# Kernel tuning notes

Measured on AMD Instinct MI355X. Metric: run time of the kernel, lower is better.

The kernel has to match this reference:

```python
import jax, jax.numpy as jnp
import numpy as np

D_IN = 2048
D_OUT = 2048
NUM_HEADS = 16
HEAD_DIM = D_OUT // NUM_HEADS


def setup_inputs() -> dict:
    key = jax.random.key(0)
    ks = jax.random.split(key, 6)
    b, t = 2, 2048
    x = jax.random.normal(ks[0], (b, t, D_IN), dtype=jnp.float32)
    s = 0.02
    Wq = jax.random.normal(ks[1], (D_OUT, D_IN), dtype=jnp.float32) * s
    Wk = jax.random.normal(ks[2], (D_OUT, D_IN), dtype=jnp.float32) * s
    Wv = jax.random.normal(ks[3], (D_OUT, D_IN), dtype=jnp.float32) * s
    Wo = jax.random.normal(ks[4], (D_OUT, D_OUT), dtype=jnp.float32) * s
    bo = jnp.zeros((D_OUT,), dtype=jnp.float32)
    theta = (10000.0 ** (-jnp.arange(0, HEAD_DIM, 2, dtype=jnp.float32) / HEAD_DIM))
    return {"x": x, "Wq": Wq, "Wk": Wk, "Wv": Wv, "Wo": Wo, "bo": bo, "theta": theta}


def _rope(v, sin, cos):
    # v: [b, t, h, d]; split even/odd feature indices, rotate, concat halves
    ve, vo = v[..., ::2], v[..., 1::2]
    return jnp.concatenate([ve * cos - vo * sin, ve * sin + vo * cos], axis=-1)


def reference(x, Wq, Wk, Wv, Wo, bo, theta):
    b, t, _ = x.shape
    q = (x @ Wq.T).reshape(b, t, NUM_HEADS, HEAD_DIM)
    k = (x @ Wk.T).reshape(b, t, NUM_HEADS, HEAD_DIM)
    v = (x @ Wv.T).reshape(b, t, NUM_HEADS, HEAD_DIM)

    pos = jnp.arange(t, dtype=jnp.float32)[:, None]          # [t, 1]
    freq = pos * theta[None, :]                              # [t, d/2]
    sin = jnp.sin(freq)[None, :, None, :]                    # [1, t, 1, d/2]
    cos = jnp.cos(freq)[None, :, None, :]
    q = _rope(q, sin, cos)
    k = _rope(k, sin, cos)

    # [b, h, t, t]
    scores = jnp.einsum('bqhd,bkhd->bhqk', q, k)
    causal = jnp.triu(jnp.ones((t, t), dtype=bool), k=1)
    scores = jnp.where(causal[None, None], -jnp.inf, scores)
    attn = jax.nn.softmax(scores / jnp.sqrt(jnp.float32(HEAD_DIM)), axis=-1)

    ctx = jnp.einsum('bhqk,bkhd->bqhd', attn, v).reshape(b, t, D_OUT)
    return ctx @ Wo.T + bo
```

## Files before the change

kernel.cpp:

```cpp
#include <hip/hip_runtime.h>

typedef unsigned short ushortT;
typedef short short8 __attribute__((ext_vector_type(8)));
typedef float floatx4 __attribute__((ext_vector_type(4)));

#define D_MODEL 2048
#define HEAD_DIM 128
#define NUM_HEADS 16
#define SEQ 2048
#define BATCH 2
#define M_TOK (BATCH * SEQ)
#define QKV_ELEMS ((size_t)M_TOK * D_MODEL)
#define W_ELEMS ((size_t)D_MODEL * D_MODEL)

__device__ __forceinline__ float bf2f(ushortT h) {
    return __uint_as_float(((unsigned int)h) << 16);
}
__device__ __forceinline__ ushortT f2bf(float f) {
    unsigned int u = __float_as_uint(f);
    u = u + 0x7fffu + ((u >> 16) & 1u);
    return (ushortT)(u >> 16);
}

__device__ __forceinline__ void gload_lds16(const ushortT* g, short* lds_wave_base) {
    __builtin_amdgcn_global_load_lds(
        (const __attribute__((address_space(1))) unsigned int*)g,
        (__attribute__((address_space(3))) unsigned int*)lds_wave_base,
        16, 0, 0);
}

__global__ __launch_bounds__(256) void cvt_all(
    const float* __restrict__ x,  const float* __restrict__ wq,
    const float* __restrict__ wk, const float* __restrict__ wv,
    const float* __restrict__ wo,
    ushortT* __restrict__ xb,  ushortT* __restrict__ wqb,
    ushortT* __restrict__ wkb, ushortT* __restrict__ wvb,
    ushortT* __restrict__ wob)
{
    const size_t XC = QKV_ELEMS / 8;
    const size_t WC = W_ELEMS / 8;
    size_t c = (size_t)blockIdx.x * 256 + threadIdx.x;
    const float* s; ushortT* d;
    if (c < XC)              { s = x;  d = xb;  }
    else if ((c -= XC) < WC) { s = wq; d = wqb; }
    else if ((c -= WC) < WC) { s = wk; d = wkb; }
    else if ((c -= WC) < WC) { s = wv; d = wvb; }
    else     { c -= WC;        s = wo; d = wob; }
    const float* f = s + c * 8;
    floatx4 a = *(const floatx4*)f;
    floatx4 b = *(const floatx4*)(f + 4);
    short8 r;
    r[0] = (short)f2bf(a.x); r[1] = (short)f2bf(a.y);
    r[2] = (short)f2bf(a.z); r[3] = (short)f2bf(a.w);
    r[4] = (short)f2bf(b.x); r[5] = (short)f2bf(b.y);
    r[6] = (short)f2bf(b.z); r[7] = (short)f2bf(b.w);
    *(short8*)(d + c * 8) = r;
}

template<bool OUTF32>
__global__ __launch_bounds__(256) void gemm_bt(
    const ushortT* __restrict__ A,
    const ushortT* __restrict__ W0, const ushortT* __restrict__ W1,
    const ushortT* __restrict__ W2,
    void* C0, void* C1, void* C2, const float* __restrict__ bias)
{
    __shared__ short As[128 * 32];
    __shared__ short Bs[128 * 32];

    const int z = blockIdx.z;
    const ushortT* W = (z == 0) ? W0 : (z == 1 ? W1 : W2);
    void* C = (z == 0) ? C0 : (z == 1 ? C1 : C2);

    const int tid  = threadIdx.x;
    const int wave = tid >> 6;
    const int lane = tid & 63;
    const int lr   = lane & 15;
    const int quad = lane >> 4;
    const int wm   = (wave & 1) * 64;
    const int wn   = (wave >> 1) * 64;

    const int blockM = blockIdx.y * 128;
    const int blockN = blockIdx.x * 128;

    const int srow = tid >> 2;
    const int scol = (tid & 3) * 8;
    const ushortT* ag = A + (size_t)(blockM + srow) * D_MODEL + scol;
    const ushortT* wg = W + (size_t)(blockN + srow) * D_MODEL + scol;
    short* al = As + wave * 512;
    short* bl = Bs + wave * 512;

    floatx4 acc[4][4];
    #pragma unroll
    for (int i = 0; i < 4; i++)
        #pragma unroll
        for (int j = 0; j < 4; j++) acc[i][j] = (floatx4){0.f, 0.f, 0.f, 0.f};

    for (int kk = 0; kk < D_MODEL; kk += 32) {
        gload_lds16(ag + kk,                 al);
        gload_lds16(ag + kk + 64 * D_MODEL,  al + 64 * 32);
        gload_lds16(wg + kk,                 bl);
        gload_lds16(wg + kk + 64 * D_MODEL,  bl + 64 * 32);
        __syncthreads();

        short8 af[4], bf[4];
        #pragma unroll
        for (int s = 0; s < 4; s++) {
            af[s] = *(const short8*)&As[(wm + s * 16 + lr) * 32 + quad * 8];
            bf[s] = *(const short8*)&Bs[(wn + s * 16 + lr) * 32 + quad * 8];
        }
        #pragma unroll
        for (int sm = 0; sm < 4; sm++)
            #pragma unroll
            for (int sn = 0; sn < 4; sn++)
                acc[sm][sn] = __builtin_amdgcn_mfma_f32_16x16x32_bf16(
                    af[sm], bf[sn], acc[sm][sn], 0, 0, 0);
        __syncthreads();
    }

    #pragma unroll
    for (int sm = 0; sm < 4; sm++) {
        const int row = blockM + wm + sm * 16 + quad * 4;
        #pragma unroll
        for (int sn = 0; sn < 4; sn++) {
            const int col = blockN + wn + sn * 16 + lr;
            const float bval = bias ? bias[col] : 0.f;
            #pragma unroll
            for (int rr = 0; rr < 4; rr++) {
                const float val = acc[sm][sn][rr] + bval;
                if constexpr (OUTF32)
                    ((float*)C)[(size_t)(row + rr) * D_MODEL + col] = val;
                else
                    ((ushortT*)C)[(size_t)(row + rr) * D_MODEL + col] = f2bf(val);
            }
        }
    }
}

__global__ __launch_bounds__(256) void rope_kernel(
    ushortT* __restrict__ qb, ushortT* __restrict__ kb,
    const float* __restrict__ theta)
{
    const int tok = blockIdx.x;
    ushortT* p = (blockIdx.y ? kb : qb) + (size_t)tok * D_MODEL;
    const int t = tok & (SEQ - 1);
    const int tid = threadIdx.x;
    const int d = tid & 63;
    const int hb = tid >> 6;

    const float fr = (float)t * theta[d];
    const float s = sinf(fr);
    const float c = cosf(fr);

    float ve[4], vo[4];
    #pragma unroll
    for (int i = 0; i < 4; i++) {
        ushortT* ph = p + (i * 4 + hb) * HEAD_DIM;
        ve[i] = bf2f(ph[2 * d]);
        vo[i] = bf2f(ph[2 * d + 1]);
    }
    __syncthreads();
    #pragma unroll
    for (int i = 0; i < 4; i++) {
        ushortT* ph = p + (i * 4 + hb) * HEAD_DIM;
        ph[d]      = f2bf(ve[i] * c - vo[i] * s);
        ph[d + 64] = f2bf(ve[i] * s + vo[i] * c);
    }
}

__global__ __launch_bounds__(256) void kpack_kernel(
    const ushortT* __restrict__ k, ushortT* __restrict__ kf)
{
    const int kt16 = blockIdx.x;
    const int bh   = blockIdx.y;
    const int b = bh >> 4, h = bh & 15;
    const int tid = threadIdx.x;
    const int ks = tid >> 6, lane = tid & 63;
    const int lr = lane & 15, quad = lane >> 4;
    short8 v = *(const short8*)(
        k + (size_t)(b * SEQ + kt16 * 16 + lr) * D_MODEL + h * HEAD_DIM + ks * 32 + quad * 8);
    *(short8*)(kf + ((size_t)(bh * 128 + kt16) * 4 + ks) * 512 + lane * 8) = v;
}

__global__ __launch_bounds__(256) void vpack_kernel(
    const ushortT* __restrict__ v, ushortT* __restrict__ vf)
{
    __shared__ ushortT tile[32][136];
    const int ct = blockIdx.x;
    const int bh = blockIdx.y;
    const int b = bh >> 4, h = bh & 15;
    const int tid = threadIdx.x;

    const int tt = tid >> 3;
    const int dc = (tid & 7) * 16;
    const ushortT* src = v + (size_t)(b * SEQ + ct * 32 + tt) * D_MODEL + h * HEAD_DIM + dc;
    *(short8*)&tile[tt][dc]     = *(const short8*)src;
    *(short8*)&tile[tt][dc + 8] = *(const short8*)(src + 8);
    __syncthreads();

    const int w = tid >> 6, lane = tid & 63;
    const int lr = lane & 15, quad = lane >> 4;
    #pragma unroll
    for (int p = 0; p < 2; p++) {
        const int rt = w + p * 4;
        short8 out;
        #pragma unroll
        for (int j = 0; j < 8; j++)
            out[j] = (short)tile[quad * 8 + j][rt * 16 + lr];
        *(short8*)(vf + ((size_t)(bh * 8 + rt) * 64 + ct) * 512 + lane * 8) = out;
    }
}

__global__ __launch_bounds__(256) void flash_attn2(
    const ushortT* __restrict__ q, const ushortT* __restrict__ kf,
    const ushortT* __restrict__ vf, ushortT* __restrict__ ctx)
{
    __shared__ short Kt[2][16 * 512];
    __shared__ short Vt[2][16 * 512];
    __shared__ short Pl[4][16][72];

    const unsigned lid = blockIdx.x;
    const int xcd  = lid & 7;
    const int slot = lid >> 3;
    const int ih   = slot >> 4;
    const int qtb  = slot & 15;
    const int bh   = (ih << 3) | xcd;

    const int b = bh >> 4, h = bh & 15;
    const size_t base = (size_t)b * SEQ * D_MODEL + h * HEAD_DIM;
    const size_t kfb = (size_t)bh * 128 * 4 * 512;
    const size_t vfb = (size_t)bh * 8 * 64 * 512;
    const int tid = threadIdx.x;
    const int w = tid >> 6, lane = tid & 63;
    const int lr = lane & 15, quad = lane >> 4;
    short* myP = &Pl[w][0][0];

    short8 onesf;
    #pragma unroll
    for (int j = 0; j < 8; j++) onesf[j] = (short)0x3F80;

    auto stage_tile = [&](int kt0, int buf) {
        const ushortT* ksrc = kf + kfb + (size_t)kt0 * 128;
        #pragma unroll
        for (int c = 0; c < 4; c++)
            gload_lds16(ksrc + c * 2048 + tid * 8, &Kt[buf][c * 2048 + w * 512]);
        #pragma unroll
        for (int c = 0; c < 4; c++) {
            const int e    = c * 2048 + tid * 8;
            const int dsub = e >> 10;
            const int rem  = e & 1023;
            const ushortT* vsrc = vf + vfb +
                ((size_t)dsub * 64 + (kt0 >> 5) + (rem >> 9)) * 512 + (rem & 511);
            gload_lds16(vsrc, &Vt[buf][c * 2048 + w * 512]);
        }
    };

    for (int pass = 0; pass < 2; pass++) {
        const int qt = (pass == 0) ? qtb : (SEQ / 64 - 1 - qtb);
        const int q0 = qt * 64 + w * 16;

        short8 Qf[4];
        {
            const ushortT* qrow = q + base + (size_t)(q0 + lr) * D_MODEL + quad * 8;
            #pragma unroll
            for (int ks = 0; ks < 4; ks++) {
                short8 raw = *(const short8*)(qrow + ks * 32);
                #pragma unroll
                for (int j = 0; j < 8; j++)
                    Qf[ks][j] = (short)f2bf(bf2f((ushortT)raw[j]) * 0.08838834764831845f);
            }
        }

        floatx4 Of[8];
        #pragma unroll
        for (int i = 0; i < 8; i++) Of[i] = (floatx4){0.f, 0.f, 0.f, 0.f};
        floatx4 lacc = (floatx4){0.f, 0.f, 0.f, 0.f};

        stage_tile(0, 0);
        asm volatile("s_waitcnt vmcnt(0)" ::: "memory");
        __builtin_amdgcn_s_barrier();
        asm volatile("" ::: "memory");

        const int ntiles = qt + 1;
        for (int t = 0; t < ntiles; ++t) {
            const int buf = t & 1;
            const int kt0 = t * 64;

            floatx4 Sf[4];
            #pragma unroll
            for (int sub = 0; sub < 4; sub++) {
                floatx4 acc = {0.f, 0.f, 0.f, 0.f};
                #pragma unroll
                for (int ks = 0; ks < 4; ks++) {
                    short8 Kf_ = *(const short8*)(&Kt[buf][(sub * 4 + ks) * 512 + lane * 8]);
                    acc = __builtin_amdgcn_mfma_f32_16x16x32_bf16(Qf[ks], Kf_, acc, 0, 0, 0);
                }
                Sf[sub] = acc;
            }

            if (kt0 == qt * 64) {
                #pragma unroll
                for (int sub = 0; sub < 4; sub++) {
                    const int ktg = kt0 + sub * 16 + lr;
                    #pragma unroll
                    for (int i = 0; i < 4; i++)
                        if (ktg > q0 + quad * 4 + i) Sf[sub][i] = -1e30f;
                }
            }

            #pragma unroll
            for (int sub = 0; sub < 4; sub++) {
                #pragma unroll
                for (int i = 0; i < 4; i++) {
                    const float p = __expf(fminf(Sf[sub][i], 60.f));
                    myP[(quad * 4 + i) * 72 + sub * 16 + lr] = (short)f2bf(p);
                }
            }

            short8 Vr[16];
            #pragma unroll
            for (int dsub = 0; dsub < 8; dsub++) {
                Vr[2 * dsub]     = *(const short8*)(&Vt[buf][dsub * 1024 + lane * 8]);
                Vr[2 * dsub + 1] = *(const short8*)(&Vt[buf][dsub * 1024 + 512 + lane * 8]);
            }

            if (t + 1 < ntiles) stage_tile((t + 1) * 64, buf ^ 1);

            asm volatile("s_waitcnt lgkmcnt(0)" ::: "memory");
            short8 Pf0 = *(const short8*)(myP + lr * 72 + quad * 8);
            short8 Pf1 = *(const short8*)(myP + lr * 72 + 32 + quad * 8);

            lacc = __builtin_amdgcn_mfma_f32_16x16x32_bf16(Pf0, onesf, lacc, 0, 0, 0);
            lacc = __builtin_amdgcn_mfma_f32_16x16x32_bf16(Pf1, onesf, lacc, 0, 0, 0);

            #pragma unroll
            for (int dsub = 0; dsub < 8; dsub++) {
                Of[dsub] = __builtin_amdgcn_mfma_f32_16x16x32_bf16(
                    Pf0, Vr[2 * dsub], Of[dsub], 0, 0, 0);
                Of[dsub] = __builtin_amdgcn_mfma_f32_16x16x32_bf16(
                    Pf1, Vr[2 * dsub + 1], Of[dsub], 0, 0, 0);
            }

            asm volatile("s_waitcnt vmcnt(0)" ::: "memory");
            __builtin_amdgcn_s_barrier();
            asm volatile("" ::: "memory");
        }

        float inv[4];
        #pragma unroll
        for (int i = 0; i < 4; i++) inv[i] = 1.f / lacc[i];
        #pragma unroll
        for (int dsub = 0; dsub < 8; dsub++)
            #pragma unroll
            for (int i = 0; i < 4; i++)
                ctx[base + (size_t)(q0 + quad * 4 + i) * D_MODEL + dsub * 16 + lr] =
                    f2bf(Of[dsub][i] * inv[i]);
    }
}

extern "C" void kernel_launch(void* const* d_in, const int* in_sizes, int n_in,
                              void* d_out, int out_size, void* d_ws, size_t ws_size,
                              hipStream_t stream) {
    const float* x     = (const float*)d_in[0];
    const float* Wq    = (const float*)d_in[1];
    const float* Wk    = (const float*)d_in[2];
    const float* Wv    = (const float*)d_in[3];
    const float* Wo    = (const float*)d_in[4];
    const float* bo    = (const float*)d_in[5];
    const float* theta = (const float*)d_in[6];

    ushortT* ws  = (ushortT*)d_ws;
    ushortT* qb  = ws;
    ushortT* kb  = ws + QKV_ELEMS;
    ushortT* vb  = ws + 2 * QKV_ELEMS;
    ushortT* kfb = ws + 3 * QKV_ELEMS;
    ushortT* xb  = kfb;
    ushortT* wqb = ws + 4 * QKV_ELEMS;
    ushortT* wkb = wqb + W_ELEMS;
    ushortT* wvb = wkb + W_ELEMS;
    ushortT* wob = wvb + W_ELEMS;

    cvt_all<<<dim3((unsigned)((QKV_ELEMS / 8 + 4 * (W_ELEMS / 8)) / 256)), 256, 0, stream>>>(
        x, Wq, Wk, Wv, Wo, xb, wqb, wkb, wvb, wob);

    gemm_bt<false><<<dim3(D_MODEL / 128, M_TOK / 128, 3), 256, 0, stream>>>(
        xb, wqb, wkb, wvb, qb, kb, vb, nullptr);

    rope_kernel<<<dim3(M_TOK, 2), 256, 0, stream>>>(qb, kb, theta);

    kpack_kernel<<<dim3(SEQ / 16, BATCH * NUM_HEADS), 256, 0, stream>>>(kb, kfb);

    vpack_kernel<<<dim3(SEQ / 32, BATCH * NUM_HEADS), 256, 0, stream>>>(vb, kb);

    flash_attn2<<<dim3(512), 256, 0, stream>>>(qb, kfb, kb, vb);

    gemm_bt<true><<<dim3(D_MODEL / 128, M_TOK / 128, 1), 256, 0, stream>>>(
        vb, wob, wob, wob, d_out, d_out, d_out, bo);
}
```

Baseline: 403.1 us.

## Fuse RoPE into K packing and Q load, write V fragments from GEMM

Removes the standalone rope and vpack kernels. RoPE is now applied to K inside kpack and to Q while flash attention loads its Q fragments, and the QKV GEMM epilogue writes V straight into the packed fragment layout. The GEMM also moves to a 64-wide K step with an XOR-swizzled LDS layout, which halves the number of barriers per K loop and is meant to reduce bank conflicts. The cost is sin/cos recomputed per element in kpack and flash attention, plus scattered 2-byte stores in the V epilogue.

Measured after the change: 441.7 us. +9.6%, slower.

```diff
diff --git a/kernel.cpp b/kernel.cpp
--- a/kernel.cpp
+++ b/kernel.cpp
@@ -57,15 +57,15 @@
     *(short8*)(d + c * 8) = r;
 }
 
-template<bool OUTF32>
+template<bool OUTF32, bool VFRAG>
 __global__ __launch_bounds__(256) void gemm_bt(
     const ushortT* __restrict__ A,
     const ushortT* __restrict__ W0, const ushortT* __restrict__ W1,
     const ushortT* __restrict__ W2,
     void* C0, void* C1, void* C2, const float* __restrict__ bias)
 {
-    __shared__ short As[128 * 32];
-    __shared__ short Bs[128 * 32];
+    __shared__ short As[128 * 64];
+    __shared__ short Bs[128 * 64];
 
     const int z = blockIdx.z;
     const ushortT* W = (z == 0) ? W0 : (z == 1 ? W1 : W2);
@@ -82,12 +82,15 @@
     const int blockM = blockIdx.y * 128;
     const int blockN = blockIdx.x * 128;
 
-    const int srow = tid >> 2;
-    const int scol = (tid & 3) * 8;
-    const ushortT* ag = A + (size_t)(blockM + srow) * D_MODEL + scol;
-    const ushortT* wg = W + (size_t)(blockN + srow) * D_MODEL + scol;
+    const int srow = tid >> 3;
+    const int scol = (tid & 7) * 8;
+    const int scolSwz = scol ^ ((srow & 7) << 3);
+    const ushortT* ag = A + (size_t)(blockM + srow) * D_MODEL + scolSwz;
+    const ushortT* wg = W + (size_t)(blockN + srow) * D_MODEL + scolSwz;
     short* al = As + wave * 512;
     short* bl = Bs + wave * 512;
+
+    const int rswz = (lr & 7) << 3;
 
     floatx4 acc[4][4];
     #pragma unroll
@@ -95,31 +98,36 @@
         #pragma unroll
         for (int j = 0; j < 4; j++) acc[i][j] = (floatx4){0.f, 0.f, 0.f, 0.f};
 
-    for (int kk = 0; kk < D_MODEL; kk += 32) {
-        gload_lds16(ag + kk,                 al);
-        gload_lds16(ag + kk + 64 * D_MODEL,  al + 64 * 32);
-        gload_lds16(wg + kk,                 bl);
-        gload_lds16(wg + kk + 64 * D_MODEL,  bl + 64 * 32);
+    for (int kk = 0; kk < D_MODEL; kk += 64) {
+        #pragma unroll
+        for (int i = 0; i < 4; i++) {
+            gload_lds16(ag + kk + (size_t)(i * 32) * D_MODEL, al + i * 2048);
+            gload_lds16(wg + kk + (size_t)(i * 32) * D_MODEL, bl + i * 2048);
+        }
         __syncthreads();
 
-        short8 af[4], bf[4];
-        #pragma unroll
-        for (int s = 0; s < 4; s++) {
-            af[s] = *(const short8*)&As[(wm + s * 16 + lr) * 32 + quad * 8];
-            bf[s] = *(const short8*)&Bs[(wn + s * 16 + lr) * 32 + quad * 8];
-        }
-        #pragma unroll
-        for (int sm = 0; sm < 4; sm++)
-            #pragma unroll
-            for (int sn = 0; sn < 4; sn++)
-                acc[sm][sn] = __builtin_amdgcn_mfma_f32_16x16x32_bf16(
-                    af[sm], bf[sn], acc[sm][sn], 0, 0, 0);
+        #pragma unroll
+        for (int kh = 0; kh < 2; kh++) {
+            const int cbase = (kh * 32 + quad * 8) ^ rswz;
+            short8 af[4], bf[4];
+            #pragma unroll
+            for (int s = 0; s < 4; s++) {
+                af[s] = *(const short8*)&As[(wm + s * 16 + lr) * 64 + cbase];
+                bf[s] = *(const short8*)&Bs[(wn + s * 16 + lr) * 64 + cbase];
+            }
+            #pragma unroll
+            for (int sm = 0; sm < 4; sm++)
+                #pragma unroll
+                for (int sn = 0; sn < 4; sn++)
+                    acc[sm][sn] = __builtin_amdgcn_mfma_f32_16x16x32_bf16(
+                        af[sm], bf[sn], acc[sm][sn], 0, 0, 0);
+        }
         __syncthreads();
     }
 
     #pragma unroll
     for (int sm = 0; sm < 4; sm++) {
-        const int row = blockM + wm + sm * 16 + quad * 4;
+        const int row0 = blockM + wm + sm * 16 + quad * 4;
         #pragma unroll
         for (int sn = 0; sn < 4; sn++) {
             const int col = blockN + wn + sn * 16 + lr;
@@ -127,48 +135,28 @@
             #pragma unroll
             for (int rr = 0; rr < 4; rr++) {
                 const float val = acc[sm][sn][rr] + bval;
-                if constexpr (OUTF32)
-                    ((float*)C)[(size_t)(row + rr) * D_MODEL + col] = val;
-                else
-                    ((ushortT*)C)[(size_t)(row + rr) * D_MODEL + col] = f2bf(val);
+                const int row = row0 + rr;
+                if (VFRAG && z == 2) {
+                    const int tt = row & (SEQ - 1);
+                    const int bh2 = ((row >> 11) << 4) | (col >> 7);
+                    const int dd = col & 127;
+                    const size_t idx =
+                        ((size_t)(bh2 * 8 + (dd >> 4)) * 64 + (tt >> 5)) * 512 +
+                        (size_t)((((tt & 31) >> 3) * 16 + (dd & 15)) * 8 + (tt & 7));
+                    ((ushortT*)C)[idx] = f2bf(val);
+                } else if constexpr (OUTF32) {
+                    ((float*)C)[(size_t)row * D_MODEL + col] = val;
+                } else {
+                    ((ushortT*)C)[(size_t)row * D_MODEL + col] = f2bf(val);
+                }
             }
         }
     }
 }
 
-__global__ __launch_bounds__(256) void rope_kernel(
-    ushortT* __restrict__ qb, ushortT* __restrict__ kb,
+__global__ __launch_bounds__(256) void kpack_kernel(
+    const ushortT* __restrict__ k, ushortT* __restrict__ kf,
     const float* __restrict__ theta)
-{
-    const int tok = blockIdx.x;
-    ushortT* p = (blockIdx.y ? kb : qb) + (size_t)tok * D_MODEL;
-    const int t = tok & (SEQ - 1);
-    const int tid = threadIdx.x;
-    const int d = tid & 63;
-    const int hb = tid >> 6;
-
-    const float fr = (float)t * theta[d];
-    const float s = sinf(fr);
-    const float c = cosf(fr);
-
-    float ve[4], vo[4];
-    #pragma unroll
-    for (int i = 0; i < 4; i++) {
-        ushortT* ph = p + (i * 4 + hb) * HEAD_DIM;
-        ve[i] = bf2f(ph[2 * d]);
-        vo[i] = bf2f(ph[2 * d + 1]);
-    }
-    __syncthreads();
-    #pragma unroll
-    for (int i = 0; i < 4; i++) {
-        ushortT* ph = p + (i * 4 + hb) * HEAD_DIM;
-        ph[d]      = f2bf(ve[i] * c - vo[i] * s);
-        ph[d + 64] = f2bf(ve[i] * s + vo[i] * c);
-    }
-}
-
-__global__ __launch_bounds__(256) void kpack_kernel(
-    const ushortT* __restrict__ k, ushortT* __restrict__ kf)
 {
     const int kt16 = blockIdx.x;
     const int bh   = blockIdx.y;
@@ -176,43 +164,31 @@
     const int tid = threadIdx.x;
     const int ks = tid >> 6, lane = tid & 63;
     const int lr = lane & 15, quad = lane >> 4;
-    short8 v = *(const short8*)(
-        k + (size_t)(b * SEQ + kt16 * 16 + lr) * D_MODEL + h * HEAD_DIM + ks * 32 + quad * 8);
+
+    const int t   = kt16 * 16 + lr;
+    const int d0  = ks * 32 + quad * 8;
+    const int dd0 = d0 & 63;
+    const ushortT* src = k + (size_t)(b * SEQ + t) * D_MODEL + h * HEAD_DIM;
+    short8 a  = *(const short8*)(src + 2 * dd0);
+    short8 b8 = *(const short8*)(src + 2 * dd0 + 8);
+    const float tp = (float)t;
+
+    short8 v;
+    #pragma unroll
+    for (int j = 0; j < 8; j++) {
+        const float ve = bf2f((ushortT)(j < 4 ? a[2 * j]     : b8[2 * j - 8]));
+        const float vo = bf2f((ushortT)(j < 4 ? a[2 * j + 1] : b8[2 * j - 7]));
+        const float ang = tp * theta[dd0 + j];
+        const float s = sinf(ang), c = cosf(ang);
+        v[j] = (short)f2bf((d0 < 64) ? (ve * c - vo * s) : (ve * s + vo * c));
+    }
     *(short8*)(kf + ((size_t)(bh * 128 + kt16) * 4 + ks) * 512 + lane * 8) = v;
-}
-
-__global__ __launch_bounds__(256) void vpack_kernel(
-    const ushortT* __restrict__ v, ushortT* __restrict__ vf)
-{
-    __shared__ ushortT tile[32][136];
-    const int ct = blockIdx.x;
-    const int bh = blockIdx.y;
-    const int b = bh >> 4, h = bh & 15;
-    const int tid = threadIdx.x;
-
-    const int tt = tid >> 3;
-    const int dc = (tid & 7) * 16;
-    const ushortT* src = v + (size_t)(b * SEQ + ct * 32 + tt) * D_MODEL + h * HEAD_DIM + dc;
-    *(short8*)&tile[tt][dc]     = *(const short8*)src;
-    *(short8*)&tile[tt][dc + 8] = *(const short8*)(src + 8);
-    __syncthreads();
-
-    const int w = tid >> 6, lane = tid & 63;
-    const int lr = lane & 15, quad = lane >> 4;
-    #pragma unroll
-    for (int p = 0; p < 2; p++) {
-        const int rt = w + p * 4;
-        short8 out;
-        #pragma unroll
-        for (int j = 0; j < 8; j++)
-            out[j] = (short)tile[quad * 8 + j][rt * 16 + lr];
-        *(short8*)(vf + ((size_t)(bh * 8 + rt) * 64 + ct) * 512 + lane * 8) = out;
-    }
 }
 
 __global__ __launch_bounds__(256) void flash_attn2(
     const ushortT* __restrict__ q, const ushortT* __restrict__ kf,
-    const ushortT* __restrict__ vf, ushortT* __restrict__ ctx)
+    const ushortT* __restrict__ vf, ushortT* __restrict__ ctx,
+    const float* __restrict__ theta)
 {
     __shared__ short Kt[2][16 * 512];
     __shared__ short Vt[2][16 * 512];
@@ -260,13 +236,23 @@
 
         short8 Qf[4];
         {
-            const ushortT* qrow = q + base + (size_t)(q0 + lr) * D_MODEL + quad * 8;
+            const ushortT* qrow = q + base + (size_t)(q0 + lr) * D_MODEL;
+            const float tp = (float)(q0 + lr);
             #pragma unroll
             for (int ks = 0; ks < 4; ks++) {
-                short8 raw = *(const short8*)(qrow + ks * 32);
-                #pragma unroll
-                for (int j = 0; j < 8; j++)
-                    Qf[ks][j] = (short)f2bf(bf2f((ushortT)raw[j]) * 0.08838834764831845f);
+                const int d0  = ks * 32 + quad * 8;
+                const int dd0 = d0 & 63;
+                short8 a  = *(const short8*)(qrow + 2 * dd0);
+                short8 b8 = *(const short8*)(qrow + 2 * dd0 + 8);
+                #pragma unroll
+                for (int j = 0; j < 8; j++) {
+                    const float ve = bf2f((ushortT)(j < 4 ? a[2 * j]     : b8[2 * j - 8]));
+                    const float vo = bf2f((ushortT)(j < 4 ? a[2 * j + 1] : b8[2 * j - 7]));
+                    const float ang = tp * theta[dd0 + j];
+                    const float s = sinf(ang), c = cosf(ang);
+                    const float r = (d0 < 64) ? (ve * c - vo * s) : (ve * s + vo * c);
+                    Qf[ks][j] = (short)f2bf(r * 0.08838834764831845f);
+                }
             }
         }
 
@@ -369,30 +355,27 @@
     const float* theta = (const float*)d_in[6];
 
     ushortT* ws  = (ushortT*)d_ws;
-    ushortT* qb  = ws;
-    ushortT* kb  = ws + QKV_ELEMS;
-    ushortT* vb  = ws + 2 * QKV_ELEMS;
-    ushortT* kfb = ws + 3 * QKV_ELEMS;
-    ushortT* xb  = kfb;
-    ushortT* wqb = ws + 4 * QKV_ELEMS;
-    ushortT* wkb = wqb + W_ELEMS;
-    ushortT* wvb = wkb + W_ELEMS;
-    ushortT* wob = wvb + W_ELEMS;
+    ushortT* qb   = ws;
+    ushortT* kb   = ws + QKV_ELEMS;
+    ushortT* vfb  = ws + 2 * QKV_ELEMS;
+    ushortT* kfbp = ws + 3 * QKV_ELEMS;
+    ushortT* xb   = kfbp;
+    ushortT* wqb  = ws + 4 * QKV_ELEMS;
+    ushortT* wkb  = wqb + W_ELEMS;
+    ushortT* wvb  = wkb + W_ELEMS;
+    ushortT* wob  = wvb + W_ELEMS;
+    ushortT* ctx  = wqb;
 
     cvt_all<<<dim3((unsigned)((QKV_ELEMS / 8 + 4 * (W_ELEMS / 8)) / 256)), 256, 0, stream>>>(
         x, Wq, Wk, Wv, Wo, xb, wqb, wkb, wvb, wob);
 
-    gemm_bt<false><<<dim3(D_MODEL / 128, M_TOK / 128, 3), 256, 0, stream>>>(
-        xb, wqb, wkb, wvb, qb, kb, vb, nullptr);
-
-    rope_kernel<<<dim3(M_TOK, 2), 256, 0, stream>>>(qb, kb, theta);
-
-    kpack_kernel<<<dim3(SEQ / 16, BATCH * NUM_HEADS), 256, 0, stream>>>(kb, kfb);
-
-    vpack_kernel<<<dim3(SEQ / 32, BATCH * NUM_HEADS), 256, 0, stream>>>(vb, kb);
-
-    flash_attn2<<<dim3(512), 256, 0, stream>>>(qb, kfb, kb, vb);
-
-    gemm_bt<true><<<dim3(D_MODEL / 128, M_TOK / 128, 1), 256, 0, stream>>>(
-        vb, wob, wob, wob, d_out, d_out, d_out, bo);
-}
+    gemm_bt<false, true><<<dim3(D_MODEL / 128, M_TOK / 128, 3), 256, 0, stream>>>(
+        xb, wqb, wkb, wvb, qb, kb, vfb, nullptr);
+
+    kpack_kernel<<<dim3(SEQ / 16, BATCH * NUM_HEADS), 256, 0, stream>>>(kb, kfbp, theta);
+
+    flash_attn2<<<dim3(512), 256, 0, stream>>>(qb, kfbp, vfb, ctx, theta);
+
+    gemm_bt<true, false><<<dim3(D_MODEL / 128, M_TOK / 128, 1), 256, 0, stream>>>(
+        ctx, wob, wob, wob, d_out, d_out, d_out, bo);
+}
```
